# Kernel optimization log

Measured on AMD Instinct MI355X. Metric: run time of the kernel, lower is better.

## Reference

```python
import math
import jax, jax.numpy as jnp
import numpy as np

B_IN, B_OUT = 32, 16
BATCH, F_IN, F_OUT = 16, 16, 64
N_ALPHA, N_BETA = 8, 4
MAX_BETA = math.pi / 8


def _wigner_d(l, betas):
    """d^l_{m',m}(beta) = <m'|exp(-i beta J_y)|m>, m ordered -l..l (quantum/CS convention)."""
    betas = np.asarray(betas, dtype=np.float64)
    if l == 0:
        return np.ones((len(betas), 1, 1))
    m = np.arange(-l, l)
    c = np.sqrt(l * (l + 1.0) - m * (m + 1.0))
    Jy = np.zeros((2 * l + 1, 2 * l + 1), dtype=np.complex128)
    i = np.arange(2 * l)
    Jy[i + 1, i] = c / 2j
    Jy[i, i + 1] = -c / 2j
    w, V = np.linalg.eigh(Jy)
    ph = np.exp(-1j * betas[:, None] * w[None, :])  # [nb, 2l+1]
    return np.einsum('mk,bk,nk->bmn', V, ph, V.conj()).real


def _quad_weights(b):
    # Driscoll-Healy quadrature weights for the 2b-point SOFT beta grid, incl. alpha weight 2pi/(2b)
    j = np.arange(2 * b)
    beta = np.pi * (2 * j + 1) / (4 * b)
    k = np.arange(b)
    s = np.sum(np.sin(beta[:, None] * (2 * k + 1)[None, :]) / (2 * k + 1)[None, :], axis=1)
    return (2.0 / b) * np.sin(beta) * s * (2.0 * np.pi / (2 * b))


def _tables():
    # S2 forward-FFT table: quadrature-weighted d^l_{m,0}(beta_j)
    betas_in = np.pi * (2 * np.arange(2 * B_IN) + 1) / (4 * B_IN)
    qw = _quad_weights(B_IN)
    nspec = B_OUT ** 2
    wig_s2 = np.zeros((2 * B_IN, nspec))
    for l in range(B_OUT):
        d = _wigner_d(l, betas_in)[:, :, l]  # d^l_{m,0}(beta_j), [2b_in, 2l+1]
        wig_s2[:, l * l:l * l + 2 * l + 1] = d * qw[:, None]
    # kernel spectral basis sampled on the (beta, alpha) grid: e^{-i m alpha} d^l_{m,0}(beta)
    gb = np.repeat((np.arange(N_BETA) + 1) * MAX_BETA / N_BETA, N_ALPHA)
    ga = np.tile(np.linspace(0, 2 * np.pi, N_ALPHA, endpoint=False), N_BETA)
    Fk = np.zeros((nspec, N_ALPHA * N_BETA), dtype=np.complex128)
    for l in range(B_OUT):
        d = _wigner_d(l, gb)[:, :, l]  # [n_grid, 2l+1]
        m = np.arange(-l, l + 1)
        Fk[l * l:l * l + 2 * l + 1] = np.exp(-1j * m[:, None] * ga[None, :]) * d.T
    # SO3 inverse-FFT table: (2l+1) * d^l_{m,n}(beta_k) on the output beta grid
    betas_out = np.pi * (2 * np.arange(2 * B_OUT) + 1) / (4 * B_OUT)
    nspec3 = sum((2 * l + 1) ** 2 for l in range(B_OUT))
    wig_so3 = np.zeros((2 * B_OUT, nspec3))
    off = 0
    for l in range(B_OUT):
        d = _wigner_d(l, betas_out)  # [2b_out, L, L]
        wig_so3[:, off:off + (2 * l + 1) ** 2] = (2 * l + 1) * d.reshape(2 * B_OUT, -1)
        off += (2 * l + 1) ** 2
    return wig_s2, Fk, wig_so3


def setup_inputs() -> dict:
    key = jax.random.key(0)
    kx, kk = jax.random.split(key)
    wig_s2, Fk, wig_so3 = _tables()
    return {
        "x": jax.random.normal(kx, (BATCH, F_IN, 2 * B_IN, 2 * B_IN), dtype=jnp.float32),
        "kernel": jax.random.uniform(kk, (F_IN, F_OUT, N_ALPHA * N_BETA), dtype=jnp.float32, minval=-1.0, maxval=1.0),
        "bias": jnp.zeros((1, F_OUT, 1, 1, 1), dtype=jnp.float32),
        "wig_s2": jnp.asarray(wig_s2, dtype=jnp.float32),
        "fk_re": jnp.asarray(Fk.real, dtype=jnp.float32),
        "fk_im": jnp.asarray(Fk.imag, dtype=jnp.float32),
        "wig_so3": jnp.asarray(wig_so3, dtype=jnp.float32),
    }


def reference(x, kernel, bias, wig_s2, fk_re, fk_im, wig_so3):
    b_in = x.shape[-1] // 2
    nspec = wig_s2.shape[1]
    b_out = int(round(math.sqrt(nspec)))
    batch, f_in = x.shape[0], x.shape[1]
    f_out, n_grid = kernel.shape[1], kernel.shape[2]
    scaling = 1.0 / math.sqrt(n_grid * f_in * b_out ** 4.0 / b_in ** 2.0)

    # --- S2 FFT: FFT over alpha, then quadrature-weighted Legendre (Wigner d_{m0}) sum over beta ---
    xf = jnp.fft.fft(x.astype(jnp.complex64), axis=-1)  # [B, Fin, 2b_in(beta), m-bins]
    m_idx = np.concatenate([np.arange(-l, l + 1) % (2 * b_in) for l in range(b_out)])  # ragged l*m layout
    fhat = jnp.einsum('bfjs,js->sbf', xf[:, :, :, m_idx], wig_s2.astype(jnp.complex64))  # [nspec, B, Fin]

    # --- s2_rft: kernel -> spherical-harmonic coefficients on the sampling grid ---
    Fk = jax.lax.complex(fk_re, fk_im)  # [nspec, n_grid]
    psi = jnp.einsum('iog,sg->sio', (kernel * scaling).astype(jnp.complex64), Fk)  # [nspec, Fin, Fout]

    # --- s2_mm (per-degree ragged block outer product) + SO3 inverse FFT ---
    spec = jnp.zeros((batch, f_out, 2 * b_out, 2 * b_out, 2 * b_out), dtype=jnp.complex64)
    off = 0
    for l in range(b_out):
        L = 2 * l + 1
        s = slice(l * l, l * l + L)
        # Fz^l_{mn} = sum_i fhat^l_m[b,i] * conj(psi^l_n[i,o])
        Fz = jnp.einsum('mbi,nio->bomn', fhat[s], jnp.conj(psi[s]))  # [B, Fout, L, L]
        d_l = wig_so3[:, off:off + L * L].reshape(2 * b_out, L, L).astype(jnp.complex64)
        mi = np.arange(-l, l + 1) % (2 * b_out)
        spec = spec.at[:, :, :, mi[:, None], mi[None, :]].add(
            jnp.einsum('bomn,kmn->bokmn', Fz, d_l))
        off += L * L
    # inverse 2D FFT over (m->alpha, n->gamma); 'forward' norm = unnormalized synthesis sum
    out = jnp.fft.ifft2(spec, axes=(-2, -1), norm='forward').real  # [B, Fout, beta, alpha, gamma]
    return out + bias
```

## Files before the change

kernel.cpp:

```cpp
#include <hip/hip_runtime.h>
#include <math.h>

#define BATCH  16
#define F_IN   16
#define F_OUT  64
#define NGRID  32
#define NSPEC  256
#define NU     136
#define NITEMS 496
#define NP4    3680
#define SCALING 0.005524271728019903f
#define PI_F 3.14159265358979323846f
#define W32 0.19634954084936207f

__device__ const int d_cof2[16] = {0,5,22,59,124,225,370,567,824,1149,1550,2035,2612,3289,4074,4975};
__device__ const int d_PB[16] = {0,16,96,240,448,652,904,1204,1552,1816,2112,2440,2800,2996,3208,3436};

__device__ __forceinline__ void decode_item(int t, int& lam, int& r, int& m, int& n) {
    lam = (int)sqrtf((float)t * 0.5f);
    while ((2*lam + 1) * (lam + 1) <= t) ++lam;
    while (lam > 0 && (2*lam - 1) * lam > t) --lam;
    r = t - (2*lam - 1) * lam;
    if (r < 2*lam + 1) { m = lam; n = r - lam; }
    else { const int r2 = r - (2*lam + 1); m = r2 >> 1; n = (r2 & 1) ? lam : -lam; }
}

__device__ __forceinline__ void decode_p4(int p4, int& l, int& m, int& n, int& valid) {
    int lam = 0;
    #pragma unroll
    for (int q = 1; q < 16; ++q) if (p4 >= d_PB[q]) lam = q;
    const int pl = (19 - lam) & ~3;
    const int q2 = p4 - d_PB[lam];
    int ti = q2 / pl;
    const int j = q2 - ti * pl;
    l = lam + j;
    valid = (j < 16 - lam);
    if (l > 15) l = 15;
    if (ti < 2*lam + 1) { m = lam; n = ti - lam; }
    else { const int r2 = ti - (2*lam + 1); m = r2 >> 1; n = (r2 & 1) ? lam : -lam; }
}

__global__ __launch_bounds__(256) void k_prep(const float* __restrict__ x,
                                              const float* __restrict__ wig_s2,
                                              const float* __restrict__ kern,
                                              const float* __restrict__ fk_re,
                                              const float* __restrict__ fk_im,
                                              const float* __restrict__ wig,
                                              float2* __restrict__ fhat,
                                              float2* __restrict__ psic,
                                              float4* __restrict__ wigt4,
                                              unsigned int* __restrict__ p4lut,
                                              unsigned int* __restrict__ itemlut) {
    __shared__ __align__(16) char smem[25088];
    const int blk = blockIdx.x;
    const int tid = threadIdx.x;

    if (blk < 256) {
        float (*xs)[65]  = (float (*)[65])smem;
        float2 (*xf)[65] = (float2 (*)[65])(smem + 16640);
        const int b = blk >> 4, f = blk & 15;

        const float4* src = (const float4*)(x + (size_t)(b * F_IN + f) * 4096);
        for (int t = tid; t < 1024; t += 256) {
            float4 v = src[t];
            const int row = t >> 4, col = (t & 15) * 4;
            xs[row][col] = v.x; xs[row][col+1] = v.y; xs[row][col+2] = v.z; xs[row][col+3] = v.w;
        }
        __syncthreads();
        {
            const int m = tid >> 4, j0 = tid & 15;
            float stc, sts;
            sincosf(-(2.f * PI_F / 64.f) * (float)m, &sts, &stc);
            float wr = 1.f, wi = 0.f;
            float ar[4] = {0,0,0,0}, ai[4] = {0,0,0,0};
            #pragma unroll 8
            for (int a = 0; a < 64; ++a) {
                #pragma unroll
                for (int q = 0; q < 4; ++q) {
                    const float v = xs[j0 + 16*q][a];
                    ar[q] += v * wr; ai[q] += v * wi;
                }
                const float nr = wr*stc - wi*sts; wi = wr*sts + wi*stc; wr = nr;
            }
            #pragma unroll
            for (int q = 0; q < 4; ++q) xf[m][j0 + 16*q] = make_float2(ar[q], ai[q]);
        }
        __syncthreads();
        if (tid < NU) {
            int l = (int)((sqrtf(8.f * (float)tid + 1.f) - 1.f) * 0.5f);
            while ((l + 1) * (l + 2) / 2 <= tid) ++l;
            while (l * (l + 1) / 2 > tid) --l;
            const int m = tid - l * (l + 1) / 2;
            const int s = l * l + l + m;
            float re = 0.f, im = 0.f;
            #pragma unroll 8
            for (int j = 0; j < 64; ++j) {
                const float2 v = xf[m][j];
                const float w = wig_s2[j * NSPEC + s];
                re += v.x * w; im += v.y * w;
            }
            fhat[(b * NU + tid) * F_IN + f] = make_float2(re, im);
        }
    } else if (blk < 512) {
        float2* fk = (float2*)smem;
        const int s = blk - 256;
        if (tid < NGRID) fk[tid] = make_float2(fk_re[s * NGRID + tid], -fk_im[s * NGRID + tid]);
        __syncthreads();
        for (int t = tid; t < F_OUT * F_IN; t += 256) {
            const int o = t >> 4, i = t & 15;
            const float4* kr = (const float4*)(kern + (size_t)(i * F_OUT + o) * NGRID);
            float re = 0.f, im = 0.f;
            #pragma unroll
            for (int g4 = 0; g4 < 8; ++g4) {
                const float4 v = kr[g4];
                const float2 a = fk[g4*4+0], b2 = fk[g4*4+1], c = fk[g4*4+2], d = fk[g4*4+3];
                re += v.x * a.x + v.y * b2.x + v.z * c.x + v.w * d.x;
                im += v.x * a.y + v.y * b2.y + v.z * c.y + v.w * d.y;
            }
            psic[(o * NSPEC + s) * F_IN + i] = make_float2(re * SCALING, im * SCALING);
        }
    } else if (blk < 627) {
        const int t = (blk - 512) * 256 + tid;
        if (t < NP4 * 8) {
            const int p4 = t >> 3, kc = t & 7;
            int l, m, n, valid;
            decode_p4(p4, l, m, n, valid);
            const int wo = d_cof2[l] + m * (2 * l + 1) + n;
            float4 v = make_float4(0.f, 0.f, 0.f, 0.f);
            if (valid) {
                v.x = wig[(kc * 4 + 0) * 5456 + wo];
                v.y = wig[(kc * 4 + 1) * 5456 + wo];
                v.z = wig[(kc * 4 + 2) * 5456 + wo];
                v.w = wig[(kc * 4 + 3) * 5456 + wo];
            }
            wigt4[(size_t)kc * NP4 + p4] = v;
            if (kc == 0) {
                const int u  = l * (l + 1) / 2 + m;
                const int sn = l * l + l + n;
                p4lut[p4] = (unsigned)u | ((unsigned)sn << 8) | ((unsigned)valid << 16);
            }
        }
    } else {
        const int t = (blk - 627) * 256 + tid;
        if (t < NITEMS) {
            int lam, r, m, n;
            decode_item(t, lam, r, m, n);
            const int pl = (19 - lam) & ~3;
            const int O4 = d_PB[lam] + r * pl;
            const int nq = pl >> 2;
            itemlut[t] = (unsigned)O4 | ((unsigned)m << 12) | ((unsigned)(n + 15) << 16) | ((unsigned)nq << 21);
        }
    }
}

__global__ __launch_bounds__(256) void k3a_fz(const float2* __restrict__ fhat,
                                              const float2* __restrict__ psic,
                                              const unsigned int* __restrict__ p4lut,
                                              float2* __restrict__ fzp) {
    __shared__ __align__(16) float2 fh[NU][18];
    __shared__ __align__(16) float2 ps[NSPEC][18];
    const int bo = blockIdx.x;
    const int b = bo >> 6, o = bo & 63;
    const int tid = threadIdx.x;

    {
        const float2* src = fhat + (size_t)b * NU * F_IN;
        for (int t = tid; t < NU * F_IN; t += 256) fh[t >> 4][t & 15] = src[t];
        const float2* src2 = psic + (size_t)o * NSPEC * F_IN;
        for (int t = tid; t < NSPEC * F_IN; t += 256) ps[t >> 4][t & 15] = src2[t];
    }
    __syncthreads();

    float2* dst = fzp + (size_t)bo * NP4;
    for (int p = tid; p < NP4; p += 256) {
        const unsigned e = p4lut[p];
        float2 outv = make_float2(0.f, 0.f);
        if (e >> 16) {
            const int u = e & 255, sn = (e >> 8) & 255;
            const float4* A4 = (const float4*)&fh[u][0];
            const float4* C4 = (const float4*)&ps[sn][0];
            float re = 0.f, im = 0.f;
            #pragma unroll
            for (int i2 = 0; i2 < 8; ++i2) {
                const float4 A = A4[i2], C = C4[i2];
                re += A.x*C.x - A.y*C.y + A.z*C.z - A.w*C.w;
                im += A.x*C.y + A.y*C.x + A.z*C.w + A.w*C.z;
            }
            outv = make_float2(re, im);
        }
        dst[p] = outv;
    }
}

__global__ __launch_bounds__(256) void k3c_main(const float2* __restrict__ fzp,
                                               const float4* __restrict__ wigt4,
                                               const unsigned int* __restrict__ itemlut,
                                               const float* __restrict__ bias,
                                               float* __restrict__ out) {
    __shared__ __align__(16) float2 S[4][16][33];
    __shared__ __align__(16) float2 G[4][16][33];
    __shared__ float2 tw[32];
    const int bo = blockIdx.x >> 3;
    const int kc = blockIdx.x & 7;
    const int tid = threadIdx.x;
    const float bb = bias[bo & 63];

    if (tid < 32) {
        float s_, c_;
        sincosf(W32 * (float)tid, &s_, &c_);
        tw[tid] = make_float2(c_, s_);
    }

    const float2* fzb = fzp + (size_t)bo * NP4;
    const float4* wtb = wigt4 + (size_t)kc * NP4;

    #pragma unroll
    for (int it = 0; it < 2; ++it) {
        const int t = tid + it * 256;
        if (t < NITEMS) {
            const unsigned e = itemlut[t];
            const int O4 = e & 0xFFF, m = (e >> 12) & 15, nn = (e >> 16) & 31, nq = (e >> 21) & 7;
            const float2* fz = fzb + O4;
            const float4* wt = wtb + O4;
            float sr0=0,si0=0,sr1=0,si1=0,sr2=0,si2=0,sr3=0,si3=0;
            for (int c = 0; c < nq; ++c) {
                #pragma unroll
                for (int j = 0; j < 4; ++j) {
                    const float2 z = fz[j];
                    const float4 w = wt[j];
                    sr0 += z.x * w.x; si0 += z.y * w.x;
                    sr1 += z.x * w.y; si1 += z.y * w.y;
                    sr2 += z.x * w.z; si2 += z.y * w.z;
                    sr3 += z.x * w.w; si3 += z.y * w.w;
                }
                fz += 4; wt += 4;
            }
            S[0][m][nn] = make_float2(sr0, si0);
            S[1][m][nn] = make_float2(sr1, si1);
            S[2][m][nn] = make_float2(sr2, si2);
            S[3][m][nn] = make_float2(sr3, si3);
        }
    }
    __syncthreads();

    {
        const int kk = tid >> 6, m = (tid >> 2) & 15, g0 = tid & 3;
        float ar[4] = {0,0,0,0}, ai[4] = {0,0,0,0}, br[4] = {0,0,0,0}, bi[4] = {0,0,0,0};
        const float2* Srow = &S[kk][m][0];
        #pragma unroll
        for (int nn = 0; nn < 31; ++nn) {
            const float2 sv = Srow[nn];
            const int n = nn - 15;
            #pragma unroll
            for (int q = 0; q < 4; ++q) {
                const int g = g0 + 4 * q;
                const float2 w = tw[(n * g) & 31];
                const float X = sv.x * w.x - sv.y * w.y;
                const float Y = sv.x * w.y + sv.y * w.x;
                ar[q] += X; ai[q] += Y;
                if (nn & 1) { br[q] += X; bi[q] += Y; }
                else        { br[q] -= X; bi[q] -= Y; }
            }
        }
        #pragma unroll
        for (int q = 0; q < 4; ++q) {
            const int g = g0 + 4 * q;
            G[kk][m][g]      = make_float2(ar[q], ai[q]);
            G[kk][m][g + 16] = make_float2(br[q], bi[q]);
        }
    }
    __syncthreads();

    {
        const int kk = tid >> 6, g = tid & 31, a0 = (tid >> 5) & 1;
        const float base = G[kk][0][g].x + bb;
        float o_[4][4];
        #pragma unroll
        for (int rep = 0; rep < 4; ++rep)
            #pragma unroll
            for (int j = 0; j < 4; ++j) o_[rep][j] = base;
        #pragma unroll
        for (int m = 1; m < 16; ++m) {
            const float2 gv = G[kk][m][g];
            const float gx = 2.f * gv.x, gy = 2.f * gv.y;
            #pragma unroll
            for (int rep = 0; rep < 4; ++rep) {
                const int A = a0 + 2 * rep;
                const float2 w = tw[(m * A) & 31];
                const float X = gx * w.x - gy * w.y;
                const float Y = gx * w.y + gy * w.x;
                o_[rep][0] += X;
                o_[rep][1] += ((m & 3) == 1) ? -Y : ((m & 3) == 2) ? -X : ((m & 3) == 3) ? Y : X;
                o_[rep][2] += (m & 1) ? -X : X;
                o_[rep][3] += ((m & 3) == 1) ? Y : ((m & 3) == 2) ? -X : ((m & 3) == 3) ? -Y : X;
            }
        }
        float* ob = out + (((size_t)bo << 15) + ((size_t)(kc * 4 + kk) << 10));
        #pragma unroll
        for (int rep = 0; rep < 4; ++rep) {
            #pragma unroll
            for (int j = 0; j < 4; ++j) {
                const int a = a0 + 2*rep + 8*j;
                ob[(a << 5) + g] = o_[rep][j];
            }
        }
    }
}

extern "C" void kernel_launch(void* const* d_in, const int* in_sizes, int n_in,
                              void* d_out, int out_size, void* d_ws, size_t ws_size,
                              hipStream_t stream) {
    const float* x       = (const float*)d_in[0];
    const float* kern    = (const float*)d_in[1];
    const float* bias    = (const float*)d_in[2];
    const float* wig_s2  = (const float*)d_in[3];
    const float* fk_re   = (const float*)d_in[4];
    const float* fk_im   = (const float*)d_in[5];
    const float* wig_so3 = (const float*)d_in[6];
    float* out = (float*)d_out;

    float2*       fhat_t  = (float2*)d_ws;
    float2*       psic_t  = (float2*)((char*)d_ws + 327680);
    float4*       wigt4   = (float4*)((char*)d_ws + 2424832);
    unsigned int* p4lut   = (unsigned int*)((char*)d_ws + 2895872);
    unsigned int* itemlut = (unsigned int*)((char*)d_ws + 2910592);
    float2*       fzp4    = (float2*)((char*)d_ws + 2912768);

    k_prep<<<629, 256, 0, stream>>>(x, wig_s2, kern, fk_re, fk_im, wig_so3,
                                    fhat_t, psic_t, wigt4, p4lut, itemlut);
    k3a_fz<<<BATCH * F_OUT, 256, 0, stream>>>(fhat_t, psic_t, p4lut, fzp4);
    k3c_main<<<BATCH * F_OUT * 8, 256, 0, stream>>>(fzp4, wigt4, itemlut, bias, out);
}
```

Baseline: 296.7 us.

## Fuse Fz computation with SO3 synthesis, keeping Fz in shared memory

Merges the Fz outer-product kernel and the SO3 inverse-transform kernel into one kernel per (batch, out-feature). Fz stays in padded shared memory instead of making a global round trip, and each block loops over the 8 beta chunks instead of launching 8 blocks. This removes the global write and read of Fz and one launch. The cost is 8x fewer blocks (1024), more shared memory per block, a serial kc loop, and fhat read straight from global memory rather than staged in LDS.

```diff
diff --git a/kernel.cpp b/kernel.cpp
--- a/kernel.cpp
+++ b/kernel.cpp
@@ -9,6 +9,7 @@
 #define NU     136
 #define NITEMS 496
 #define NP4    3680
+#define NP4Q   3910
 #define SCALING 0.005524271728019903f
 #define PI_F 3.14159265358979323846f
 #define W32 0.19634954084936207f
@@ -153,57 +154,20 @@
     }
 }
 
-__global__ __launch_bounds__(256) void k3a_fz(const float2* __restrict__ fhat,
-                                              const float2* __restrict__ psic,
-                                              const unsigned int* __restrict__ p4lut,
-                                              float2* __restrict__ fzp) {
-    __shared__ __align__(16) float2 fh[NU][18];
-    __shared__ __align__(16) float2 ps[NSPEC][18];
+__global__ __launch_bounds__(256) void k3b_fused(const float2* __restrict__ fhat,
+                                                 const float2* __restrict__ psic,
+                                                 const float4* __restrict__ wigt4,
+                                                 const unsigned int* __restrict__ p4lut,
+                                                 const unsigned int* __restrict__ itemlut,
+                                                 const float* __restrict__ bias,
+                                                 float* __restrict__ out) {
+    __shared__ __align__(16) float2 fzL[NP4Q];
+    __shared__ __align__(16) char sgbuf[36864];
+    __shared__ float2 tw[32];
     const int bo = blockIdx.x;
     const int b = bo >> 6, o = bo & 63;
     const int tid = threadIdx.x;
-
-    {
-        const float2* src = fhat + (size_t)b * NU * F_IN;
-        for (int t = tid; t < NU * F_IN; t += 256) fh[t >> 4][t & 15] = src[t];
-        const float2* src2 = psic + (size_t)o * NSPEC * F_IN;
-        for (int t = tid; t < NSPEC * F_IN; t += 256) ps[t >> 4][t & 15] = src2[t];
-    }
-    __syncthreads();
-
-    float2* dst = fzp + (size_t)bo * NP4;
-    for (int p = tid; p < NP4; p += 256) {
-        const unsigned e = p4lut[p];
-        float2 outv = make_float2(0.f, 0.f);
-        if (e >> 16) {
-            const int u = e & 255, sn = (e >> 8) & 255;
-            const float4* A4 = (const float4*)&fh[u][0];
-            const float4* C4 = (const float4*)&ps[sn][0];
-            float re = 0.f, im = 0.f;
-            #pragma unroll
-            for (int i2 = 0; i2 < 8; ++i2) {
-                const float4 A = A4[i2], C = C4[i2];
-                re += A.x*C.x - A.y*C.y + A.z*C.z - A.w*C.w;
-                im += A.x*C.y + A.y*C.x + A.z*C.w + A.w*C.z;
-            }
-            outv = make_float2(re, im);
-        }
-        dst[p] = outv;
-    }
-}
-
-__global__ __launch_bounds__(256) void k3c_main(const float2* __restrict__ fzp,
-                                               const float4* __restrict__ wigt4,
-                                               const unsigned int* __restrict__ itemlut,
-                                               const float* __restrict__ bias,
-                                               float* __restrict__ out) {
-    __shared__ __align__(16) float2 S[4][16][33];
-    __shared__ __align__(16) float2 G[4][16][33];
-    __shared__ float2 tw[32];
-    const int bo = blockIdx.x >> 3;
-    const int kc = blockIdx.x & 7;
-    const int tid = threadIdx.x;
-    const float bb = bias[bo & 63];
+    const float bb = bias[o];
 
     if (tid < 32) {
         float s_, c_;
@@ -211,97 +175,135 @@
         tw[tid] = make_float2(c_, s_);
     }
 
-    const float2* fzb = fzp + (size_t)bo * NP4;
-    const float4* wtb = wigt4 + (size_t)kc * NP4;
-
-    #pragma unroll
-    for (int it = 0; it < 2; ++it) {
-        const int t = tid + it * 256;
-        if (t < NITEMS) {
-            const unsigned e = itemlut[t];
-            const int O4 = e & 0xFFF, m = (e >> 12) & 15, nn = (e >> 16) & 31, nq = (e >> 21) & 7;
-            const float2* fz = fzb + O4;
-            const float4* wt = wtb + O4;
-            float sr0=0,si0=0,sr1=0,si1=0,sr2=0,si2=0,sr3=0,si3=0;
-            for (int c = 0; c < nq; ++c) {
-                #pragma unroll
-                for (int j = 0; j < 4; ++j) {
-                    const float2 z = fz[j];
-                    const float4 w = wt[j];
-                    sr0 += z.x * w.x; si0 += z.y * w.x;
-                    sr1 += z.x * w.y; si1 += z.y * w.y;
-                    sr2 += z.x * w.z; si2 += z.y * w.z;
-                    sr3 += z.x * w.w; si3 += z.y * w.w;
-                }
-                fz += 4; wt += 4;
-            }
-            S[0][m][nn] = make_float2(sr0, si0);
-            S[1][m][nn] = make_float2(sr1, si1);
-            S[2][m][nn] = make_float2(sr2, si2);
-            S[3][m][nn] = make_float2(sr3, si3);
+    float2* psL = (float2*)sgbuf;
+    {
+        const float4* src = (const float4*)(psic + (size_t)o * NSPEC * F_IN);
+        for (int t = tid; t < 2048; t += 256) {
+            const int row = t >> 3, c4 = t & 7;
+            *(float4*)(psL + row * 18 + c4 * 2) = src[t];
         }
     }
     __syncthreads();
 
     {
-        const int kk = tid >> 6, m = (tid >> 2) & 15, g0 = tid & 3;
-        float ar[4] = {0,0,0,0}, ai[4] = {0,0,0,0}, br[4] = {0,0,0,0}, bi[4] = {0,0,0,0};
-        const float2* Srow = &S[kk][m][0];
+        const float2* fhb = fhat + (size_t)b * NU * F_IN;
+        for (int p = tid; p < NP4; p += 256) {
+            const unsigned e = p4lut[p];
+            float2 v = make_float2(0.f, 0.f);
+            if (e >> 16) {
+                const int u = e & 255, sn = (e >> 8) & 255;
+                const float4* A4 = (const float4*)(fhb + u * 16);
+                const float4* C4 = (const float4*)(psL + sn * 18);
+                float re = 0.f, im = 0.f;
+                #pragma unroll
+                for (int i2 = 0; i2 < 8; ++i2) {
+                    const float4 A = A4[i2], C = C4[i2];
+                    re += A.x*C.x - A.y*C.y + A.z*C.z - A.w*C.w;
+                    im += A.x*C.y + A.y*C.x + A.z*C.w + A.w*C.z;
+                }
+                v = make_float2(re, im);
+            }
+            fzL[p + (p >> 4)] = v;
+        }
+    }
+    __syncthreads();
+
+    float2 (*S)[16][33] = (float2 (*)[16][33])sgbuf;
+    float2 (*G)[16][33] = (float2 (*)[16][33])(sgbuf + 16896);
+
+    for (int kc = 0; kc < 8; ++kc) {
+        const float4* wtb = wigt4 + (size_t)kc * NP4;
+
         #pragma unroll
-        for (int nn = 0; nn < 31; ++nn) {
-            const float2 sv = Srow[nn];
-            const int n = nn - 15;
+        for (int it = 0; it < 2; ++it) {
+            const int t = tid + it * 256;
+            if (t < NITEMS) {
+                const unsigned e = itemlut[t];
+                const int O4 = e & 0xFFF, m = (e >> 12) & 15, nn = (e >> 16) & 31, nq = (e >> 21) & 7;
+                const float4* wt = wtb + O4;
+                float sr0=0,si0=0,sr1=0,si1=0,sr2=0,si2=0,sr3=0,si3=0;
+                int idx = O4;
+                for (int c = 0; c < nq; ++c) {
+                    #pragma unroll
+                    for (int j = 0; j < 4; ++j) {
+                        const int q = idx + j;
+                        const float2 z = fzL[q + (q >> 4)];
+                        const float4 w = wt[c * 4 + j];
+                        sr0 += z.x * w.x; si0 += z.y * w.x;
+                        sr1 += z.x * w.y; si1 += z.y * w.y;
+                        sr2 += z.x * w.z; si2 += z.y * w.z;
+                        sr3 += z.x * w.w; si3 += z.y * w.w;
+                    }
+                    idx += 4;
+                }
+                S[0][m][nn] = make_float2(sr0, si0);
+                S[1][m][nn] = make_float2(sr1, si1);
+                S[2][m][nn] = make_float2(sr2, si2);
+                S[3][m][nn] = make_float2(sr3, si3);
+            }
+        }
+        __syncthreads();
+
+        {
+            const int kk = tid >> 6, m = (tid >> 2) & 15, g0 = tid & 3;
+            float ar[4] = {0,0,0,0}, ai[4] = {0,0,0,0}, br[4] = {0,0,0,0}, bi[4] = {0,0,0,0};
+            const float2* Srow = &S[kk][m][0];
+            #pragma unroll
+            for (int nn = 0; nn < 31; ++nn) {
+                const float2 sv = Srow[nn];
+                const int n = nn - 15;
+                #pragma unroll
+                for (int q = 0; q < 4; ++q) {
+                    const int g = g0 + 4 * q;
+                    const float2 w = tw[(n * g) & 31];
+                    const float X = sv.x * w.x - sv.y * w.y;
+                    const float Y = sv.x * w.y + sv.y * w.x;
+                    ar[q] += X; ai[q] += Y;
+                    if (nn & 1) { br[q] += X; bi[q] += Y; }
+                    else        { br[q] -= X; bi[q] -= Y; }
+                }
+            }
             #pragma unroll
             for (int q = 0; q < 4; ++q) {
                 const int g = g0 + 4 * q;
-                const float2 w = tw[(n * g) & 31];
-                const float X = sv.x * w.x - sv.y * w.y;
-                const float Y = sv.x * w.y + sv.y * w.x;
-                ar[q] += X; ai[q] += Y;
-                if (nn & 1) { br[q] += X; bi[q] += Y; }
-                else        { br[q] -= X; bi[q] -= Y; }
-            }
-        }
-        #pragma unroll
-        for (int q = 0; q < 4; ++q) {
-            const int g = g0 + 4 * q;
-            G[kk][m][g]      = make_float2(ar[q], ai[q]);
-            G[kk][m][g + 16] = make_float2(br[q], bi[q]);
-        }
-    }
-    __syncthreads();
-
-    {
-        const int kk = tid >> 6, g = tid & 31, a0 = (tid >> 5) & 1;
-        const float base = G[kk][0][g].x + bb;
-        float o_[4][4];
-        #pragma unroll
-        for (int rep = 0; rep < 4; ++rep)
-            #pragma unroll
-            for (int j = 0; j < 4; ++j) o_[rep][j] = base;
-        #pragma unroll
-        for (int m = 1; m < 16; ++m) {
-            const float2 gv = G[kk][m][g];
-            const float gx = 2.f * gv.x, gy = 2.f * gv.y;
+                G[kk][m][g]      = make_float2(ar[q], ai[q]);
+                G[kk][m][g + 16] = make_float2(br[q], bi[q]);
+            }
+        }
+        __syncthreads();
+
+        {
+            const int kk = tid >> 6, g = tid & 31, a0 = (tid >> 5) & 1;
+            const float base = G[kk][0][g].x + bb;
+            float o_[4][4];
+            #pragma unroll
+            for (int rep = 0; rep < 4; ++rep)
+                #pragma unroll
+                for (int j = 0; j < 4; ++j) o_[rep][j] = base;
+            #pragma unroll
+            for (int m = 1; m < 16; ++m) {
+                const float2 gv = G[kk][m][g];
+                const float gx = 2.f * gv.x, gy = 2.f * gv.y;
+                #pragma unroll
+                for (int rep = 0; rep < 4; ++rep) {
+                    const int A = a0 + 2 * rep;
+                    const float2 w = tw[(m * A) & 31];
+                    const float X = gx * w.x - gy * w.y;
+                    const float Y = gx * w.y + gy * w.x;
+                    o_[rep][0] += X;
+                    o_[rep][1] += ((m & 3) == 1) ? -Y : ((m & 3) == 2) ? -X : ((m & 3) == 3) ? Y : X;
+                    o_[rep][2] += (m & 1) ? -X : X;
+                    o_[rep][3] += ((m & 3) == 1) ? Y : ((m & 3) == 2) ? -X : ((m & 3) == 3) ? -Y : X;
+                }
+            }
+            float* ob = out + (((size_t)bo << 15) + ((size_t)(kc * 4 + kk) << 10));
             #pragma unroll
             for (int rep = 0; rep < 4; ++rep) {
-                const int A = a0 + 2 * rep;
-                const float2 w = tw[(m * A) & 31];
-                const float X = gx * w.x - gy * w.y;
-                const float Y = gx * w.y + gy * w.x;
-                o_[rep][0] += X;
-                o_[rep][1] += ((m & 3) == 1) ? -Y : ((m & 3) == 2) ? -X : ((m & 3) == 3) ? Y : X;
-                o_[rep][2] += (m & 1) ? -X : X;
-                o_[rep][3] += ((m & 3) == 1) ? Y : ((m & 3) == 2) ? -X : ((m & 3) == 3) ? -Y : X;
-            }
-        }
-        float* ob = out + (((size_t)bo << 15) + ((size_t)(kc * 4 + kk) << 10));
-        #pragma unroll
-        for (int rep = 0; rep < 4; ++rep) {
-            #pragma unroll
-            for (int j = 0; j < 4; ++j) {
-                const int a = a0 + 2*rep + 8*j;
-                ob[(a << 5) + g] = o_[rep][j];
+                #pragma unroll
+                for (int j = 0; j < 4; ++j) {
+                    const int a = a0 + 2*rep + 8*j;
+                    ob[(a << 5) + g] = o_[rep][j];
+                }
             }
         }
     }
@@ -324,10 +326,8 @@
     float4*       wigt4   = (float4*)((char*)d_ws + 2424832);
     unsigned int* p4lut   = (unsigned int*)((char*)d_ws + 2895872);
     unsigned int* itemlut = (unsigned int*)((char*)d_ws + 2910592);
-    float2*       fzp4    = (float2*)((char*)d_ws + 2912768);
 
     k_prep<<<629, 256, 0, stream>>>(x, wig_s2, kern, fk_re, fk_im, wig_so3,
                                     fhat_t, psic_t, wigt4, p4lut, itemlut);
-    k3a_fz<<<BATCH * F_OUT, 256, 0, stream>>>(fhat_t, psic_t, p4lut, fzp4);
-    k3c_main<<<BATCH * F_OUT * 8, 256, 0, stream>>>(fzp4, wigt4, itemlut, bias, out);
-}
+    k3b_fused<<<BATCH * F_OUT, 256, 0, stream>>>(fhat_t, psic_t, wigt4, p4lut, itemlut, bias, out);
+}
```

New measurement: 427.1 us. 1.44x slower.
